# Optimization experiments

Measured on AMD Instinct MI355X. Metric: run time of the kernel, lower is better.

## Reference

```python
import jax, jax.numpy as jnp
import numpy as np

DIM = 128
NUM_HEADS = 4
WIN = 16  # effective window: window_size(8) * sqrt(dim_t=4)
N = WIN * WIN
B_ = 512
NW = 64


def _relative_position_index(wh, ww):
    coords = np.stack(np.meshgrid(np.arange(wh), np.arange(ww), indexing='ij'))  # (2,wh,ww)
    cf = coords.reshape(2, -1)
    rel = cf[:, :, None] - cf[:, None, :]  # (2,N,N)
    rel = rel.transpose(1, 2, 0).copy()
    rel[:, :, 0] += wh - 1
    rel[:, :, 1] += ww - 1
    rel[:, :, 0] *= 2 * ww - 1
    return rel.sum(-1).astype(np.int32)  # (N,N)


def setup_inputs() -> dict:
    key = jax.random.key(0)
    ks = jax.random.split(key, 7)
    inputs = jax.random.normal(ks[0], (B_, N, DIM), dtype=jnp.float32)
    mask = jax.random.normal(ks[1], (NW, N, N), dtype=jnp.float32)
    qkv_w = jax.random.normal(ks[2], (3 * DIM, DIM), dtype=jnp.float32) * 0.02
    qkv_b = jnp.zeros((3 * DIM,), dtype=jnp.float32)
    proj_w = jax.random.normal(ks[3], (DIM, DIM), dtype=jnp.float32) * 0.02
    proj_b = jnp.zeros((DIM,), dtype=jnp.float32)
    table_sz = (2 * WIN - 1) * (2 * WIN - 1)  # 961
    bias_table = jax.random.normal(ks[4], (table_sz, NUM_HEADS), dtype=jnp.float32) * 0.02
    rel_idx = jnp.asarray(_relative_position_index(WIN, WIN))  # (N,N) int32
    return {"inputs": inputs, "mask": mask, "qkv_w": qkv_w, "qkv_b": qkv_b,
            "proj_w": proj_w, "proj_b": proj_b, "bias_table": bias_table,
            "rel_idx": rel_idx}


def reference(inputs, mask, qkv_w, qkv_b, proj_w, proj_b, bias_table, rel_idx):
    B, Nn, C = inputs.shape
    H = bias_table.shape[1]
    Dh = C // H
    scale = Dh ** -0.5
    qkv = (inputs @ qkv_w.T + qkv_b).reshape(B, Nn, 3, H, Dh)
    qkv = jnp.transpose(qkv, (2, 0, 3, 1, 4))  # (3,B,H,N,Dh)
    q, k, v = qkv[0] * scale, qkv[1], qkv[2]
    attn = jnp.einsum('bhnd,bhmd->bhnm', q, k)  # (B,H,N,N)
    rpb = jnp.transpose(bias_table[rel_idx], (2, 0, 1))  # (H,N,N)
    attn = attn + rpb[None]
    nW = mask.shape[0]
    attn = attn.reshape(B // nW, nW, H, Nn, Nn) + mask[None, :, None]
    attn = jax.nn.softmax(attn.reshape(B, H, Nn, Nn), axis=-1)
    out = jnp.einsum('bhnm,bhmd->bhnd', attn, v)
    out = jnp.transpose(out, (0, 2, 1, 3)).reshape(B, Nn, C)
    return out @ proj_w.T + proj_b
```

## Files before the change

kernel.cpp:

```cpp
#include <hip/hip_runtime.h>

typedef __bf16 bf16;
typedef __bf16 bf16x8 __attribute__((ext_vector_type(8)));
typedef __bf16 bf16x4 __attribute__((ext_vector_type(4)));
typedef float f32x4 __attribute__((ext_vector_type(4)));

static __device__ __forceinline__ f32x4 mfma16(bf16x8 a, bf16x8 b, f32x4 c) {
  return __builtin_amdgcn_mfma_f32_16x16x32_bf16(a, b, c, 0, 0, 0);
}

static __device__ __forceinline__ bf16x8 ld_bf8(const float* __restrict__ p) {
  f32x4 a = *(const f32x4*)p;
  f32x4 b = *(const f32x4*)(p + 4);
  bf16x8 r;
  r[0] = (bf16)a[0]; r[1] = (bf16)a[1]; r[2] = (bf16)a[2]; r[3] = (bf16)a[3];
  r[4] = (bf16)b[0]; r[5] = (bf16)b[1]; r[6] = (bf16)b[2]; r[7] = (bf16)b[3];
  return r;
}

__global__ void k0_rpb(const float* __restrict__ bt, const int* __restrict__ ri,
                       float* __restrict__ rpb) {
  int t = blockIdx.x * 256 + threadIdx.x;
  int idx = ri[t];
  f32x4 v = *(const f32x4*)(bt + idx * 4);
#pragma unroll
  for (int h = 0; h < 4; ++h) rpb[h * 65536 + t] = v[h];
}

__global__ void __launch_bounds__(256, 2)
k1_qkv(const float* __restrict__ x, const float* __restrict__ qw,
       const float* __restrict__ qb, bf16* __restrict__ q_s,
       bf16* __restrict__ k_s, bf16* __restrict__ vt) {
  const int tid = threadIdx.x;
  const int wv = tid >> 6, ln = tid & 15, qd = (tid >> 4) & 3;
  const int b = blockIdx.x >> 1;
  const int row0 = (blockIdx.x & 1) * 128 + (wv >> 1) * 64;
  const int cg = wv & 1;

  bf16x8 xf[4][4];
#pragma unroll
  for (int nt = 0; nt < 4; ++nt)
#pragma unroll
    for (int ks = 0; ks < 4; ++ks)
      xf[nt][ks] = ld_bf8(x + (size_t)(b * 256 + row0 + nt * 16 + ln) * 128 +
                          ks * 32 + qd * 8);

#pragma unroll
  for (int ch = 0; ch < 2; ++ch) {
    f32x4 acc[4][4];
#pragma unroll
    for (int mt = 0; mt < 4; ++mt)
#pragma unroll
      for (int nt = 0; nt < 4; ++nt) acc[mt][nt] = (f32x4){0.f, 0.f, 0.f, 0.f};
#pragma unroll
    for (int mt = 0; mt < 4; ++mt)
#pragma unroll
      for (int ks = 0; ks < 4; ++ks) {
        bf16x8 wf = ld_bf8(qw + (size_t)(ch * 128 + cg * 64 + mt * 16 + ln) * 128 +
                           ks * 32 + qd * 8);
#pragma unroll
        for (int nt = 0; nt < 4; ++nt) acc[mt][nt] = mfma16(wf, xf[nt][ks], acc[mt][nt]);
      }
    bf16* dst = ch ? k_s : q_s;
    const float scl = ch ? 1.0f : 0.17677669529663689f;
#pragma unroll
    for (int mt = 0; mt < 4; ++mt) {
      const int c0 = cg * 64 + mt * 16 + qd * 4;
      f32x4 b4 = *(const f32x4*)(qb + ch * 128 + c0);
      const int hh = c0 >> 5, d0 = c0 & 31;
#pragma unroll
      for (int nt = 0; nt < 4; ++nt) {
        const int nr = row0 + nt * 16 + ln;
        bf16x4 o;
#pragma unroll
        for (int r = 0; r < 4; ++r) o[r] = (bf16)((acc[mt][nt][r] + b4[r]) * scl);
        *(bf16x4*)(dst + (size_t)((b * 4 + hh) * 256 + nr) * 32 + d0) = o;
      }
    }
  }

  f32x4 av[4][4];
#pragma unroll
  for (int nt = 0; nt < 4; ++nt)
#pragma unroll
    for (int mt = 0; mt < 4; ++mt) av[nt][mt] = (f32x4){0.f, 0.f, 0.f, 0.f};
#pragma unroll
  for (int ks = 0; ks < 4; ++ks)
#pragma unroll
    for (int mt = 0; mt < 4; ++mt) {
      bf16x8 wf = ld_bf8(qw + (size_t)(256 + cg * 64 + mt * 16 + ln) * 128 +
                         ks * 32 + qd * 8);
#pragma unroll
      for (int nt = 0; nt < 4; ++nt) av[nt][mt] = mfma16(xf[nt][ks], wf, av[nt][mt]);
    }
#pragma unroll
  for (int nt = 0; nt < 4; ++nt)
#pragma unroll
    for (int mt = 0; mt < 4; ++mt) {
      const int c = cg * 64 + mt * 16 + ln;
      const float bb = qb[256 + c];
      const int hh = c >> 5, dd = c & 31;
      const int n0 = row0 + nt * 16 + qd * 4;
      bf16x4 o;
#pragma unroll
      for (int r = 0; r < 4; ++r) o[r] = (bf16)(av[nt][mt][r] + bb);
      *(bf16x4*)(vt + (size_t)((b * 4 + hh) * 32 + dd) * 256 + n0) = o;
    }
}

__global__ void __launch_bounds__(256, 2)
k2_attn(const bf16* __restrict__ q_s, const bf16* __restrict__ k_s,
        const bf16* __restrict__ vt, const float* __restrict__ mask,
        const float* __restrict__ rpb, float* __restrict__ ao) {
  __shared__ bf16 ksm[256 * 32];
  __shared__ bf16 vsm[32 * 256];
  __shared__ bf16 psm[4 * 16 * 256];
  const int tid = threadIdx.x, wv = tid >> 6;
  const int ln = tid & 15, qd = (tid >> 4) & 3;
  const int w = blockIdx.x & 63, h = (blockIdx.x >> 6) & 3, rh = blockIdx.x >> 8;

  bf16x4 cmb[2][16];
#pragma unroll
  for (int si = 0; si < 2; ++si) {
    const int n = (rh * 8 + wv * 2 + si) * 16 + ln;
#pragma unroll
    for (int mt = 0; mt < 16; ++mt) {
      f32x4 m4 = *(const f32x4*)(mask + (size_t)(w * 256 + n) * 256 + mt * 16 + qd * 4);
      f32x4 r4 = *(const f32x4*)(rpb + (size_t)h * 65536 + n * 256 + mt * 16 + qd * 4);
      bf16x4 cv;
#pragma unroll
      for (int r = 0; r < 4; ++r) cv[r] = (bf16)(m4[r] + r4[r]);
      cmb[si][mt] = cv;
    }
  }

  for (int ib = 0; ib < 8; ++ib) {
    const int b = w + ib * 64;
    const bf16* kp = k_s + (size_t)(b * 4 + h) * 8192;
    const bf16* vp = vt + (size_t)(b * 4 + h) * 8192;
    __syncthreads();
#pragma unroll
    for (int i = 0; i < 4; ++i) {
      const int ci = i * 256 + tid;
      {
        const int r_ = ci >> 2, cb = ci & 3;
        *(bf16x8*)(ksm + r_ * 32 + ((cb ^ (r_ & 3)) * 8)) =
            *(const bf16x8*)(kp + r_ * 32 + cb * 8);
      }
      {
        const int r_ = ci >> 5, cb = ci & 31;
        *(bf16x8*)(vsm + r_ * 256 + ((cb ^ (r_ & 7)) * 8)) =
            *(const bf16x8*)(vp + r_ * 256 + cb * 8);
      }
    }
    __syncthreads();

#pragma unroll
    for (int si = 0; si < 2; ++si) {
      const int s = rh * 8 + wv * 2 + si;
      bf16x8 qf = *(const bf16x8*)(q_s + (size_t)(b * 4 + h) * 8192 +
                                   (s * 16 + ln) * 32 + qd * 8);
      f32x4 acc[16];
#pragma unroll
      for (int mt = 0; mt < 16; ++mt) acc[mt] = (f32x4){0.f, 0.f, 0.f, 0.f};
#pragma unroll
      for (int mt = 0; mt < 16; ++mt) {
        const int m = mt * 16 + ln;
        bf16x8 af = *(const bf16x8*)(ksm + m * 32 + ((qd ^ (m & 3)) * 8));
        acc[mt] = mfma16(af, qf, acc[mt]);
      }
      float sum = 0.f;
      bf16* pb = psm + wv * 4096 + ln * 256;
#pragma unroll
      for (int mt = 0; mt < 16; ++mt) {
        bf16x4 pv;
#pragma unroll
        for (int r = 0; r < 4; ++r) {
          float p = __expf(acc[mt][r] + (float)cmb[si][mt][r]);
          sum += p;
          pv[r] = (bf16)p;
        }
        *(bf16x4*)(pb + (((mt * 2 + (qd >> 1)) ^ (ln & 7)) * 8) + (qd & 1) * 4) = pv;
      }
      sum += __shfl_xor(sum, 16);
      sum += __shfl_xor(sum, 32);
      const float linv = 1.0f / sum;

      f32x4 accO[2];
      accO[0] = (f32x4){0.f, 0.f, 0.f, 0.f};
      accO[1] = (f32x4){0.f, 0.f, 0.f, 0.f};
#pragma unroll
      for (int kt = 0; kt < 8; ++kt) {
        bf16x8 pf = *(const bf16x8*)(pb + (((kt * 4 + qd) ^ (ln & 7)) * 8));
#pragma unroll
        for (int ct = 0; ct < 2; ++ct) {
          const int d = ct * 16 + ln;
          bf16x8 vf = *(const bf16x8*)(vsm + d * 256 + (((kt * 4 + qd) ^ (d & 7)) * 8));
          accO[ct] = mfma16(pf, vf, accO[ct]);
        }
      }
#pragma unroll
      for (int r = 0; r < 4; ++r) {
        const float lb = __shfl(linv, qd * 4 + r);
        const size_t orow = (size_t)(b * 256 + s * 16 + qd * 4 + r) * 128 + h * 32;
#pragma unroll
        for (int ct = 0; ct < 2; ++ct)
          ao[orow + ct * 16 + ln] = accO[ct][r] * lb;
      }
    }
  }
}

__global__ void __launch_bounds__(256, 2)
k3_proj(const float* __restrict__ xin, const float* __restrict__ pw,
        const float* __restrict__ pbias, float* __restrict__ out) {
  const int tid = threadIdx.x;
  const int wv = tid >> 6, ln = tid & 15, qd = (tid >> 4) & 3;
  const int cg = wv & 1;
  const size_t row0 = (size_t)blockIdx.x * 128 + (wv >> 1) * 64;

  bf16x8 xf[4][4];
#pragma unroll
  for (int nt = 0; nt < 4; ++nt)
#pragma unroll
    for (int ks = 0; ks < 4; ++ks)
      xf[nt][ks] = ld_bf8(xin + (row0 + nt * 16 + ln) * 128 + ks * 32 + qd * 8);
  __syncthreads();

  f32x4 acc[4][4];
#pragma unroll
  for (int mt = 0; mt < 4; ++mt)
#pragma unroll
    for (int nt = 0; nt < 4; ++nt) acc[mt][nt] = (f32x4){0.f, 0.f, 0.f, 0.f};
#pragma unroll
  for (int mt = 0; mt < 4; ++mt)
#pragma unroll
    for (int ks = 0; ks < 4; ++ks) {
      bf16x8 wf = ld_bf8(pw + (size_t)(cg * 64 + mt * 16 + ln) * 128 + ks * 32 + qd * 8);
#pragma unroll
      for (int nt = 0; nt < 4; ++nt) acc[mt][nt] = mfma16(wf, xf[nt][ks], acc[mt][nt]);
    }
#pragma unroll
  for (int mt = 0; mt < 4; ++mt) {
    const int c0 = cg * 64 + mt * 16 + qd * 4;
    f32x4 b4 = *(const f32x4*)(pbias + c0);
#pragma unroll
    for (int nt = 0; nt < 4; ++nt) {
      f32x4 o;
#pragma unroll
      for (int r = 0; r < 4; ++r) o[r] = acc[mt][nt][r] + b4[r];
      *(f32x4*)(out + (row0 + nt * 16 + ln) * 128 + c0) = o;
    }
  }
}

extern "C" void kernel_launch(void* const* d_in, const int* in_sizes, int n_in,
                              void* d_out, int out_size, void* d_ws, size_t ws_size,
                              hipStream_t stream) {
  const float* x = (const float*)d_in[0];
  const float* mask = (const float*)d_in[1];
  const float* qkv_w = (const float*)d_in[2];
  const float* qkv_b = (const float*)d_in[3];
  const float* proj_w = (const float*)d_in[4];
  const float* proj_b = (const float*)d_in[5];
  const float* bias_table = (const float*)d_in[6];
  const int* rel_idx = (const int*)d_in[7];

  char* ws = (char*)d_ws;
  bf16* q_s = (bf16*)ws;
  bf16* k_s = (bf16*)(ws + 33554432);
  bf16* vt = (bf16*)(ws + 2ll * 33554432);
  float* rpb = (float*)(ws + 3ll * 33554432);
  float* ao = (float*)d_out;

  k0_rpb<<<dim3(256), dim3(256), 0, stream>>>(bias_table, rel_idx, rpb);
  k1_qkv<<<dim3(1024), dim3(256), 0, stream>>>(x, qkv_w, qkv_b, q_s, k_s, vt);
  k2_attn<<<dim3(512), dim3(256), 0, stream>>>(q_s, k_s, vt, mask, rpb, ao);
  k3_proj<<<dim3(1024), dim3(256), 0, stream>>>(ao, proj_w, proj_b, (float*)d_out);
}
```

Baseline: 307.6 us.

## Read K/V from global directly, double attention grid, store bf16 intermediate

The attention kernel no longer stages K and V into shared memory. Each wave reads its fragments straight from global or cache, and the block barriers are removed. Each block now covers 4 query strips instead of 8, so the grid doubles to 1024 blocks and the launch bound rises to 4 blocks per SM. The attention output is written in bf16 to workspace when the workspace is large enough, which halves the traffic between the attention and projection kernels, at the cost of uncoalesced global reads for K/V and one extra bf16 rounding.

```diff
diff --git a/kernel.cpp b/kernel.cpp
--- a/kernel.cpp
+++ b/kernel.cpp
@@ -108,111 +108,94 @@
     }
 }
 
-__global__ void __launch_bounds__(256, 2)
+__global__ void __launch_bounds__(256, 4)
 k2_attn(const bf16* __restrict__ q_s, const bf16* __restrict__ k_s,
         const bf16* __restrict__ vt, const float* __restrict__ mask,
-        const float* __restrict__ rpb, float* __restrict__ ao) {
-  __shared__ bf16 ksm[256 * 32];
-  __shared__ bf16 vsm[32 * 256];
+        const float* __restrict__ rpb, float* __restrict__ aof,
+        bf16* __restrict__ aob, const int use_bf) {
   __shared__ bf16 psm[4 * 16 * 256];
   const int tid = threadIdx.x, wv = tid >> 6;
   const int ln = tid & 15, qd = (tid >> 4) & 3;
-  const int w = blockIdx.x & 63, h = (blockIdx.x >> 6) & 3, rh = blockIdx.x >> 8;
-
-  bf16x4 cmb[2][16];
-#pragma unroll
-  for (int si = 0; si < 2; ++si) {
-    const int n = (rh * 8 + wv * 2 + si) * 16 + ln;
-#pragma unroll
-    for (int mt = 0; mt < 16; ++mt) {
-      f32x4 m4 = *(const f32x4*)(mask + (size_t)(w * 256 + n) * 256 + mt * 16 + qd * 4);
-      f32x4 r4 = *(const f32x4*)(rpb + (size_t)h * 65536 + n * 256 + mt * 16 + qd * 4);
-      bf16x4 cv;
-#pragma unroll
-      for (int r = 0; r < 4; ++r) cv[r] = (bf16)(m4[r] + r4[r]);
-      cmb[si][mt] = cv;
-    }
-  }
+  const int w = blockIdx.x & 63, h = (blockIdx.x >> 6) & 3, rr = blockIdx.x >> 8;
+  const int s = rr * 4 + wv;
+  const int n = s * 16 + ln;
+
+  bf16x4 cmb[16];
+#pragma unroll
+  for (int mt = 0; mt < 16; ++mt) {
+    f32x4 m4 = *(const f32x4*)(mask + (size_t)(w * 256 + n) * 256 + mt * 16 + qd * 4);
+    f32x4 r4 = *(const f32x4*)(rpb + (size_t)h * 65536 + n * 256 + mt * 16 + qd * 4);
+    bf16x4 cv;
+#pragma unroll
+    for (int r = 0; r < 4; ++r) cv[r] = (bf16)(m4[r] + r4[r]);
+    cmb[mt] = cv;
+  }
+
+  bf16* pb = psm + wv * 4096 + ln * 256;
 
   for (int ib = 0; ib < 8; ++ib) {
     const int b = w + ib * 64;
-    const bf16* kp = k_s + (size_t)(b * 4 + h) * 8192;
-    const bf16* vp = vt + (size_t)(b * 4 + h) * 8192;
-    __syncthreads();
-#pragma unroll
-    for (int i = 0; i < 4; ++i) {
-      const int ci = i * 256 + tid;
-      {
-        const int r_ = ci >> 2, cb = ci & 3;
-        *(bf16x8*)(ksm + r_ * 32 + ((cb ^ (r_ & 3)) * 8)) =
-            *(const bf16x8*)(kp + r_ * 32 + cb * 8);
-      }
-      {
-        const int r_ = ci >> 5, cb = ci & 31;
-        *(bf16x8*)(vsm + r_ * 256 + ((cb ^ (r_ & 7)) * 8)) =
-            *(const bf16x8*)(vp + r_ * 256 + cb * 8);
-      }
-    }
-    __syncthreads();
-
-#pragma unroll
-    for (int si = 0; si < 2; ++si) {
-      const int s = rh * 8 + wv * 2 + si;
-      bf16x8 qf = *(const bf16x8*)(q_s + (size_t)(b * 4 + h) * 8192 +
-                                   (s * 16 + ln) * 32 + qd * 8);
-      f32x4 acc[16];
-#pragma unroll
-      for (int mt = 0; mt < 16; ++mt) acc[mt] = (f32x4){0.f, 0.f, 0.f, 0.f};
-#pragma unroll
-      for (int mt = 0; mt < 16; ++mt) {
-        const int m = mt * 16 + ln;
-        bf16x8 af = *(const bf16x8*)(ksm + m * 32 + ((qd ^ (m & 3)) * 8));
-        acc[mt] = mfma16(af, qf, acc[mt]);
-      }
-      float sum = 0.f;
-      bf16* pb = psm + wv * 4096 + ln * 256;
-#pragma unroll
-      for (int mt = 0; mt < 16; ++mt) {
-        bf16x4 pv;
-#pragma unroll
-        for (int r = 0; r < 4; ++r) {
-          float p = __expf(acc[mt][r] + (float)cmb[si][mt][r]);
-          sum += p;
-          pv[r] = (bf16)p;
-        }
-        *(bf16x4*)(pb + (((mt * 2 + (qd >> 1)) ^ (ln & 7)) * 8) + (qd & 1) * 4) = pv;
-      }
-      sum += __shfl_xor(sum, 16);
-      sum += __shfl_xor(sum, 32);
-      const float linv = 1.0f / sum;
-
-      f32x4 accO[2];
-      accO[0] = (f32x4){0.f, 0.f, 0.f, 0.f};
-      accO[1] = (f32x4){0.f, 0.f, 0.f, 0.f};
-#pragma unroll
-      for (int kt = 0; kt < 8; ++kt) {
-        bf16x8 pf = *(const bf16x8*)(pb + (((kt * 4 + qd) ^ (ln & 7)) * 8));
-#pragma unroll
-        for (int ct = 0; ct < 2; ++ct) {
-          const int d = ct * 16 + ln;
-          bf16x8 vf = *(const bf16x8*)(vsm + d * 256 + (((kt * 4 + qd) ^ (d & 7)) * 8));
-          accO[ct] = mfma16(pf, vf, accO[ct]);
-        }
-      }
+    const size_t base = (size_t)(b * 4 + h) * 8192;
+    const bf16* kp = k_s + base;
+    const bf16* vp = vt + base;
+    bf16x8 qf = *(const bf16x8*)(q_s + base + (size_t)n * 32 + qd * 8);
+
+    f32x4 acc[16];
+#pragma unroll
+    for (int mt = 0; mt < 16; ++mt) acc[mt] = (f32x4){0.f, 0.f, 0.f, 0.f};
+#pragma unroll
+    for (int mt = 0; mt < 16; ++mt) {
+      bf16x8 af = *(const bf16x8*)(kp + (mt * 16 + ln) * 32 + qd * 8);
+      acc[mt] = mfma16(af, qf, acc[mt]);
+    }
+    float sum = 0.f;
+#pragma unroll
+    for (int mt = 0; mt < 16; ++mt) {
+      bf16x4 pv;
 #pragma unroll
       for (int r = 0; r < 4; ++r) {
-        const float lb = __shfl(linv, qd * 4 + r);
-        const size_t orow = (size_t)(b * 256 + s * 16 + qd * 4 + r) * 128 + h * 32;
+        float p = __expf(acc[mt][r] + (float)cmb[mt][r]);
+        sum += p;
+        pv[r] = (bf16)p;
+      }
+      *(bf16x4*)(pb + (((mt * 2 + (qd >> 1)) ^ (ln & 7)) * 8) + (qd & 1) * 4) = pv;
+    }
+    sum += __shfl_xor(sum, 16);
+    sum += __shfl_xor(sum, 32);
+    const float linv = 1.0f / sum;
+
+    f32x4 accO[2];
+    accO[0] = (f32x4){0.f, 0.f, 0.f, 0.f};
+    accO[1] = (f32x4){0.f, 0.f, 0.f, 0.f};
+#pragma unroll
+    for (int kt = 0; kt < 8; ++kt) {
+      bf16x8 pf = *(const bf16x8*)(pb + (((kt * 4 + qd) ^ (ln & 7)) * 8));
+#pragma unroll
+      for (int ct = 0; ct < 2; ++ct) {
+        const int d = ct * 16 + ln;
+        bf16x8 vf = *(const bf16x8*)(vp + d * 256 + kt * 32 + qd * 8);
+        accO[ct] = mfma16(pf, vf, accO[ct]);
+      }
+    }
+#pragma unroll
+    for (int r = 0; r < 4; ++r) {
+      const float lb = __shfl(linv, qd * 4 + r);
+      const size_t orow = (size_t)(b * 256 + s * 16 + qd * 4 + r) * 128 + h * 32;
+      if (use_bf) {
 #pragma unroll
         for (int ct = 0; ct < 2; ++ct)
-          ao[orow + ct * 16 + ln] = accO[ct][r] * lb;
+          aob[orow + ct * 16 + ln] = (bf16)(accO[ct][r] * lb);
+      } else {
+#pragma unroll
+        for (int ct = 0; ct < 2; ++ct) aof[orow + ct * 16 + ln] = accO[ct][r] * lb;
       }
     }
   }
 }
 
 __global__ void __launch_bounds__(256, 2)
-k3_proj(const float* __restrict__ xin, const float* __restrict__ pw,
+k3_proj(const float* __restrict__ xf32, const bf16* __restrict__ xb16,
+        const int use_bf, const float* __restrict__ pw,
         const float* __restrict__ pbias, float* __restrict__ out) {
   const int tid = threadIdx.x;
   const int wv = tid >> 6, ln = tid & 15, qd = (tid >> 4) & 3;
@@ -223,8 +206,13 @@
 #pragma unroll
   for (int nt = 0; nt < 4; ++nt)
 #pragma unroll
-    for (int ks = 0; ks < 4; ++ks)
-      xf[nt][ks] = ld_bf8(xin + (row0 + nt * 16 + ln) * 128 + ks * 32 + qd * 8);
+    for (int ks = 0; ks < 4; ++ks) {
+      const size_t off = (row0 + nt * 16 + ln) * 128 + ks * 32 + qd * 8;
+      if (use_bf)
+        xf[nt][ks] = *(const bf16x8*)(xb16 + off);
+      else
+        xf[nt][ks] = ld_bf8(xf32 + off);
+    }
   __syncthreads();
 
   f32x4 acc[4][4];
@@ -271,10 +259,14 @@
   bf16* k_s = (bf16*)(ws + 33554432);
   bf16* vt = (bf16*)(ws + 2ll * 33554432);
   float* rpb = (float*)(ws + 3ll * 33554432);
-  float* ao = (float*)d_out;
+  const size_t WS_NEED = 3ull * 33554432 + 1048576 + 33554432;
+  const int use_bf = (ws_size >= WS_NEED) ? 1 : 0;
+  bf16* aob = (bf16*)(ws + 3ll * 33554432 + 1048576);
+  float* aof = (float*)d_out;
 
   k0_rpb<<<dim3(256), dim3(256), 0, stream>>>(bias_table, rel_idx, rpb);
   k1_qkv<<<dim3(1024), dim3(256), 0, stream>>>(x, qkv_w, qkv_b, q_s, k_s, vt);
-  k2_attn<<<dim3(512), dim3(256), 0, stream>>>(q_s, k_s, vt, mask, rpb, ao);
-  k3_proj<<<dim3(1024), dim3(256), 0, stream>>>(ao, proj_w, proj_b, (float*)d_out);
-}
+  k2_attn<<<dim3(1024), dim3(256), 0, stream>>>(q_s, k_s, vt, mask, rpb, aof, aob, use_bf);
+  k3_proj<<<dim3(1024), dim3(256), 0, stream>>>(aof, aob, use_bf, proj_w, proj_b,
+                                                (float*)d_out);
+}
```

Result: slower. 401.7 us (+30.6%).

## Store attention output and mask/bias intermediates in bf16 to cut traffic

Applied to the files above, without the earlier changes.

A new prep kernel converts the window mask and the gathered relative-position bias to bf16 once per call, and stores them in the output buffer as scratch. The attention kernel then reads half-width mask and bias data. It writes its normalized output as bf16 in a head-major layout, reusing the Q buffer in place instead of writing fp32 rows. The projection kernel reads that bf16 tensor directly, dropping the fp32-to-bf16 conversion and a barrier. This cuts global memory traffic for the intermediates, at the cost of an extra full pass over the mask and the mask being rounded to bf16 before the bias is added.

```diff
diff --git a/kernel.cpp b/kernel.cpp
--- a/kernel.cpp
+++ b/kernel.cpp
@@ -18,13 +18,21 @@
   return r;
 }
 
-__global__ void k0_rpb(const float* __restrict__ bt, const int* __restrict__ ri,
-                       float* __restrict__ rpb) {
+__global__ void k0_prep(const float* __restrict__ mask, const float* __restrict__ bt,
+                        const int* __restrict__ ri, bf16* __restrict__ mb,
+                        bf16* __restrict__ rb) {
   int t = blockIdx.x * 256 + threadIdx.x;
-  int idx = ri[t];
-  f32x4 v = *(const f32x4*)(bt + idx * 4);
-#pragma unroll
-  for (int h = 0; h < 4; ++h) rpb[h * 65536 + t] = v[h];
+  f32x4 m4 = *(const f32x4*)(mask + (size_t)t * 4);
+  bf16x4 o;
+#pragma unroll
+  for (int r = 0; r < 4; ++r) o[r] = (bf16)m4[r];
+  *(bf16x4*)(mb + (size_t)t * 4) = o;
+  if (t < 65536) {
+    int idx = ri[t];
+    f32x4 v = *(const f32x4*)(bt + idx * 4);
+#pragma unroll
+    for (int h = 0; h < 4; ++h) rb[h * 65536 + t] = (bf16)v[h];
+  }
 }
 
 __global__ void __launch_bounds__(256, 2)
@@ -109,9 +117,9 @@
 }
 
 __global__ void __launch_bounds__(256, 2)
-k2_attn(const bf16* __restrict__ q_s, const bf16* __restrict__ k_s,
-        const bf16* __restrict__ vt, const float* __restrict__ mask,
-        const float* __restrict__ rpb, float* __restrict__ ao) {
+k2_attn(bf16* __restrict__ q_s, const bf16* __restrict__ k_s,
+        const bf16* __restrict__ vt, const bf16* __restrict__ mb,
+        const bf16* __restrict__ rb) {
   __shared__ bf16 ksm[256 * 32];
   __shared__ bf16 vsm[32 * 256];
   __shared__ bf16 psm[4 * 16 * 256];
@@ -125,11 +133,11 @@
     const int n = (rh * 8 + wv * 2 + si) * 16 + ln;
 #pragma unroll
     for (int mt = 0; mt < 16; ++mt) {
-      f32x4 m4 = *(const f32x4*)(mask + (size_t)(w * 256 + n) * 256 + mt * 16 + qd * 4);
-      f32x4 r4 = *(const f32x4*)(rpb + (size_t)h * 65536 + n * 256 + mt * 16 + qd * 4);
+      bf16x4 m4 = *(const bf16x4*)(mb + (size_t)(w * 256 + n) * 256 + mt * 16 + qd * 4);
+      bf16x4 r4 = *(const bf16x4*)(rb + (size_t)h * 65536 + n * 256 + mt * 16 + qd * 4);
       bf16x4 cv;
 #pragma unroll
-      for (int r = 0; r < 4; ++r) cv[r] = (bf16)(m4[r] + r4[r]);
+      for (int r = 0; r < 4; ++r) cv[r] = (bf16)((float)m4[r] + (float)r4[r]);
       cmb[si][mt] = cv;
     }
   }
@@ -202,17 +210,18 @@
 #pragma unroll
       for (int r = 0; r < 4; ++r) {
         const float lb = __shfl(linv, qd * 4 + r);
-        const size_t orow = (size_t)(b * 256 + s * 16 + qd * 4 + r) * 128 + h * 32;
+        const size_t obase =
+            (size_t)(b * 4 + h) * 8192 + (size_t)(s * 16 + qd * 4 + r) * 32;
 #pragma unroll
         for (int ct = 0; ct < 2; ++ct)
-          ao[orow + ct * 16 + ln] = accO[ct][r] * lb;
+          q_s[obase + ct * 16 + ln] = (bf16)(accO[ct][r] * lb);
       }
     }
   }
 }
 
 __global__ void __launch_bounds__(256, 2)
-k3_proj(const float* __restrict__ xin, const float* __restrict__ pw,
+k3_proj(const bf16* __restrict__ xb, const float* __restrict__ pw,
         const float* __restrict__ pbias, float* __restrict__ out) {
   const int tid = threadIdx.x;
   const int wv = tid >> 6, ln = tid & 15, qd = (tid >> 4) & 3;
@@ -221,11 +230,13 @@
 
   bf16x8 xf[4][4];
 #pragma unroll
-  for (int nt = 0; nt < 4; ++nt)
+  for (int nt = 0; nt < 4; ++nt) {
+    const size_t row = row0 + nt * 16 + ln;
+    const size_t b = row >> 8, n = row & 255;
 #pragma unroll
     for (int ks = 0; ks < 4; ++ks)
-      xf[nt][ks] = ld_bf8(xin + (row0 + nt * 16 + ln) * 128 + ks * 32 + qd * 8);
-  __syncthreads();
+      xf[nt][ks] = *(const bf16x8*)(xb + ((b * 4 + ks) * 256 + n) * 32 + qd * 8);
+  }
 
   f32x4 acc[4][4];
 #pragma unroll
@@ -270,11 +281,11 @@
   bf16* q_s = (bf16*)ws;
   bf16* k_s = (bf16*)(ws + 33554432);
   bf16* vt = (bf16*)(ws + 2ll * 33554432);
-  float* rpb = (float*)(ws + 3ll * 33554432);
-  float* ao = (float*)d_out;
-
-  k0_rpb<<<dim3(256), dim3(256), 0, stream>>>(bias_table, rel_idx, rpb);
+  bf16* mb = (bf16*)d_out;
+  bf16* rb = (bf16*)((char*)d_out + 16777216);
+
+  k0_prep<<<dim3(4096), dim3(256), 0, stream>>>(mask, bias_table, rel_idx, mb, rb);
   k1_qkv<<<dim3(1024), dim3(256), 0, stream>>>(x, qkv_w, qkv_b, q_s, k_s, vt);
-  k2_attn<<<dim3(512), dim3(256), 0, stream>>>(q_s, k_s, vt, mask, rpb, ao);
-  k3_proj<<<dim3(1024), dim3(256), 0, stream>>>(ao, proj_w, proj_b, (float*)d_out);
-}
+  k2_attn<<<dim3(512), dim3(256), 0, stream>>>(q_s, k_s, vt, mb, rb);
+  k3_proj<<<dim3(1024), dim3(256), 0, stream>>>(q_s, proj_w, proj_b, (float*)d_out);
+}
```

Result: no change. 308.9 us (+0.4%).
